# Kernel tuning notes

Measured on AMD Instinct MI355X. Metric: run time of the kernel, lower is better.

## Reference

```python
import jax, jax.numpy as jnp
import numpy as np

N = 12000   # atoms per side
K = 32      # neighbors per point per radius
E = N * K   # edges per radius
R = 1500    # residues per side
P = 4096    # correspondence pairs
LN_EPS = 1e-5


def setup_inputs() -> dict:
    rng = np.random.default_rng(0)

    def unit(v):
        return (v / np.linalg.norm(v, axis=-1, keepdims=True)).astype(np.float32)

    pos_A = (rng.standard_normal((N, 3)) * 10.0).astype(np.float32)
    pos_B = (rng.standard_normal((N, 3)) * 10.0).astype(np.float32)
    normal_A = unit(rng.standard_normal((N, 3)))
    normal_B = unit(rng.standard_normal((N, 3)))

    def make_edges():
        dst = np.repeat(np.arange(N), K)                      # every node is a target
        src = (dst + 1 + rng.integers(0, N - 1, size=dst.shape)) % N  # src != dst
        return np.stack([src, dst]).astype(np.int32)          # [2, E]

    edges_A = np.stack([make_edges() for _ in range(3)])      # [3, 2, E]
    edges_B = np.stack([make_edges() for _ in range(3)])

    residue_idx_A = (np.arange(N) // (N // R)).astype(np.int32)
    residue_idx_B = (np.arange(N) // (N // R)).astype(np.int32)
    src_idx = rng.integers(0, R, P).astype(np.int32)
    tgt_idx = rng.integers(0, R, P).astype(np.int32)

    g = lambda *s: (rng.standard_normal(s) * 0.2).astype(np.float32)
    inp = dict(
        pos_A=jnp.asarray(pos_A), normal_A=jnp.asarray(normal_A),
        pos_B=jnp.asarray(pos_B), normal_B=jnp.asarray(normal_B),
        edges_A=jnp.asarray(edges_A), edges_B=jnp.asarray(edges_B),
        residue_idx_A=jnp.asarray(residue_idx_A), residue_idx_B=jnp.asarray(residue_idx_B),
        src_idx=jnp.asarray(src_idx), tgt_idx=jnp.asarray(tgt_idx),
        num_res=R,
        conv_w1=jnp.asarray(g(3, 4, 4)), conv_b1=jnp.zeros((3, 4), jnp.float32),
        conv_g1=jnp.ones((3, 4), jnp.float32), conv_be1=jnp.zeros((3, 4), jnp.float32),
        conv_w2=jnp.asarray(g(3, 4, 128)), conv_b2=jnp.zeros((3, 128), jnp.float32),
        conv_g2=jnp.ones((3, 128), jnp.float32), conv_be2=jnp.zeros((3, 128), jnp.float32),
        atom_w=jnp.asarray(g(384, 512)) * 0.25, atom_b=jnp.zeros((512,), jnp.float32),
        atom_g=jnp.ones((512,), jnp.float32), atom_be=jnp.zeros((512,), jnp.float32),
        res_w=jnp.asarray(g(512, 512)) * 0.25, res_b=jnp.zeros((512,), jnp.float32),
        res_g=jnp.ones((512,), jnp.float32), res_be=jnp.zeros((512,), jnp.float32),
        lin1_w=jnp.asarray(g(512, 1)), lin1_b=jnp.zeros((1,), jnp.float32),
    )
    return inp


def _mlp_layer(x, w, b, g, be):
    # Seq(Linear, ReLU, LayerNorm, Dropout(eval)) from MLP()
    h = jax.nn.relu(x @ w + b)
    mu = jnp.mean(h, axis=-1, keepdims=True)
    var = jnp.mean((h - mu) ** 2, axis=-1, keepdims=True)
    return g * (h - mu) * jax.lax.rsqrt(var + LN_EPS) + be


def _angle(v1, v2):
    c = jnp.cross(v1, v2)
    return jnp.arctan2(jnp.linalg.norm(c, axis=-1), jnp.sum(v1 * v2, axis=-1))


def _ppf(pos, normal, src, dst):
    # PyG point_pair_features: [||d||, <(n_i,d), <(n_j,d), <(n_i,n_j)], d = pos_j - pos_i
    d = pos[src] - pos[dst]
    dist = jnp.linalg.norm(d, axis=-1)
    n_i, n_j = normal[dst], normal[src]
    return jnp.stack([dist, _angle(n_i, d), _angle(n_j, d), _angle(n_i, n_j)], axis=-1)  # [E,4]


def reference(pos_A, normal_A, pos_B, normal_B, edges_A, edges_B,
              residue_idx_A, residue_idx_B, src_idx, tgt_idx, num_res,
              conv_w1, conv_b1, conv_g1, conv_be1, conv_w2, conv_b2, conv_g2, conv_be2,
              atom_w, atom_b, atom_g, atom_be, res_w, res_b, res_g, res_be,
              lin1_w, lin1_b):
    n = pos_A.shape[0]

    def side(pos, normal, edges):
        feats = []
        for r in range(3):  # conv2, conv3, conv4 (shared across A/B sides)
            src, dst = edges[r, 0], edges[r, 1]
            f = _ppf(pos, normal, src, dst)                         # [E,4]
            h = _mlp_layer(f, conv_w1[r], conv_b1[r], conv_g1[r], conv_be1[r])
            h = _mlp_layer(h, conv_w2[r], conv_b2[r], conv_g2[r], conv_be2[r])  # [E,128]
            feats.append(jax.ops.segment_max(h, dst, num_segments=n))          # [N,128]
        x = jnp.concatenate(feats, axis=-1)                         # [N,384]
        return _mlp_layer(x, atom_w, atom_b, atom_g, atom_be)       # [N,512]

    atom_x_A = side(pos_A, normal_A, edges_A)
    atom_x_B = side(pos_B, normal_B, edges_B)

    res_x_A = jax.ops.segment_max(atom_x_A, residue_idx_A, num_segments=num_res)
    res_x_B = jax.ops.segment_max(atom_x_B, residue_idx_B, num_segments=num_res)
    res_x_A = _mlp_layer(res_x_A, res_w, res_b, res_g, res_be)
    res_x_B = _mlp_layer(res_x_B, res_w, res_b, res_g, res_be)

    x_s = res_x_A[src_idx]
    x_t = res_x_B[tgt_idx]
    out = (x_s - x_t) @ lin1_w + lin1_b                              # [P,1]
    return jax.nn.sigmoid(out)
```

## Files before the change

kernel.cpp:

```cpp
#include <hip/hip_runtime.h>
#include <hip/hip_bf16.h>
#include <math.h>

#define N_ATOMS 12000
#define K_NB 32
#define E_EDGES (N_ATOMS*K_NB)
#define R_RES 1500
#define P_PAIRS 4096
#define LN_EPS 1e-5f

typedef __attribute__((ext_vector_type(8))) short short8;
typedef __attribute__((ext_vector_type(4))) float f32x4;
typedef __attribute__((ext_vector_type(4))) unsigned int u32x4;

__device__ __forceinline__ f32x4 splat4(float v){ f32x4 r = {v,v,v,v}; return r; }

__device__ __forceinline__ unsigned short f2bf(float f){
  unsigned u = __builtin_bit_cast(unsigned, f);
  u += 0x7FFF + ((u >> 16) & 1);
  return (unsigned short)(u >> 16);
}

template<int CTRL>
__device__ __forceinline__ float dpp_add(float v){
  int x = __builtin_amdgcn_mov_dpp(__builtin_bit_cast(int, v), CTRL, 0xf, 0xf, true);
  return v + __builtin_bit_cast(float, x);
}
__device__ __forceinline__ float dpp16sum(float v){
  v = dpp_add<0xB1>(v);
  v = dpp_add<0x4E>(v);
  v = dpp_add<0x141>(v);
  v = dpp_add<0x140>(v);
  return v;
}

__device__ __forceinline__ float fast_atan2(float y, float x){
  float ax = fabsf(x);
  float mn = fminf(ax, y);
  float mx = fmaxf(fmaxf(ax, y), 1e-30f);
  float r  = __builtin_amdgcn_rcpf(mx);
  r = r * (2.0f - mx * r);
  float a = mn * r;
  float s = a * a;
  float p = -0.0117212f;
  p = fmaf(p, s,  0.05265332f);
  p = fmaf(p, s, -0.11643287f);
  p = fmaf(p, s,  0.19354346f);
  p = fmaf(p, s, -0.33262347f);
  p = fmaf(p, s,  0.99997726f);
  p = p * a;
  p = (y > ax) ? (1.57079632679f - p) : p;
  p = (x < 0.f) ? (3.14159265359f - p) : p;
  return p;
}

__device__ __forceinline__ float angle3(float ax,float ay,float az,
                                        float bx,float by,float bz){
  float cx = ay*bz - az*by;
  float cy = az*bx - ax*bz;
  float cz = ax*by - ay*bx;
  float cn = sqrtf(cx*cx + cy*cy + cz*cz);
  float dt = ax*bx + ay*by + az*bz;
  return fast_atan2(cn, dt);
}

__global__ __launch_bounds__(256) void geom_wpack_kernel(
    const float* __restrict__ pos_A, const float* __restrict__ nrm_A,
    const float* __restrict__ pos_B, const float* __restrict__ nrm_B,
    const int* __restrict__ edges_A, const int* __restrict__ edges_B,
    const float* __restrict__ w1, const float* __restrict__ b1,
    const float* __restrict__ g1, const float* __restrict__ be1,
    unsigned short* __restrict__ a_rec,
    const float* __restrict__ atom_w, const float* __restrict__ res_w,
    unsigned short* __restrict__ wpA, unsigned short* __restrict__ wpB)
{
  const int bx = blockIdx.x;
  const int r = blockIdx.y;
  const int side = blockIdx.z;

  if (bx >= 1500) {
    int fb = (r*2 + side)*299 + (bx - 1500);
    if (fb < 768) {
      int idx = fb*256 + threadIdx.x;
      int k = idx >> 9, n = idx & 511;
      wpA[(size_t)(k>>5)*512*32 + n*32 + (k&31)] = f2bf(atom_w[idx]);
    } else if (fb < 1792) {
      int idx = (fb - 768)*256 + threadIdx.x;
      int k = idx >> 9, n = idx & 511;
      wpB[(size_t)(k>>5)*512*32 + n*32 + (k&31)] = f2bf(res_w[idx]);
    }
    return;
  }

  const float* __restrict__ pos = side ? pos_B : pos_A;
  const float* __restrict__ nrm = side ? nrm_B : nrm_A;
  const int* __restrict__ edges = (side ? edges_B : edges_A) + r*(2*E_EDGES);

  const int e = bx*256 + threadIdx.x;
  const int src = edges[e];
  const int dst = e >> 5;

  float psx = pos[src*3+0], psy = pos[src*3+1], psz = pos[src*3+2];
  float pdx = pos[dst*3+0], pdy = pos[dst*3+1], pdz = pos[dst*3+2];
  float dx = psx-pdx, dy = psy-pdy, dz = psz-pdz;
  float nix = nrm[dst*3+0], niy = nrm[dst*3+1], niz = nrm[dst*3+2];
  float njx = nrm[src*3+0], njy = nrm[src*3+1], njz = nrm[src*3+2];

  float f0 = sqrtf(dx*dx + dy*dy + dz*dz);
  float f1 = angle3(nix,niy,niz, dx,dy,dz);
  float f2 = angle3(njx,njy,njz, dx,dy,dz);
  float f3 = angle3(nix,niy,niz, njx,njy,njz);

  const float* w1r  = w1 + r*16;
  const float* b1r  = b1 + r*4;
  const float* g1r  = g1 + r*4;
  const float* be1r = be1 + r*4;
  float h[4]; float s1 = 0.f;
  #pragma unroll
  for (int j = 0; j < 4; ++j) {
    float t = b1r[j] + f0*w1r[j] + f1*w1r[4+j] + f2*w1r[8+j] + f3*w1r[12+j];
    t = fmaxf(t, 0.f);
    h[j] = t; s1 += t;
  }
  float mu1 = s1*0.25f;
  float v1 = 0.f;
  #pragma unroll
  for (int j = 0; j < 4; ++j) { float d = h[j]-mu1; v1 += d*d; }
  float inv1 = rsqrtf(v1*0.25f + LN_EPS);
  float a0 = g1r[0]*(h[0]-mu1)*inv1 + be1r[0];
  float a1 = g1r[1]*(h[1]-mu1)*inv1 + be1r[1];
  float a2 = g1r[2]*(h[2]-mu1)*inv1 + be1r[2];
  float a3 = g1r[3]*(h[3]-mu1)*inv1 + be1r[3];

  ushort4 rec;
  rec.x = f2bf(a0); rec.y = f2bf(a1); rec.z = f2bf(a2); rec.w = f2bf(a3);
  *(ushort4*)(a_rec + ((size_t)(side*3+r)*E_EDGES + e)*4) = rec;
}

__global__ __launch_bounds__(256) void edge_gemm_kernel(
    const unsigned short* __restrict__ a_rec,
    const float* __restrict__ w2, const float* __restrict__ b2,
    const float* __restrict__ g2, const float* __restrict__ be2,
    unsigned short* __restrict__ feats_A, unsigned short* __restrict__ feats_B)
{
  const int r = blockIdx.y;
  const int side = blockIdx.z;
  unsigned short* __restrict__ feats = side ? feats_B : feats_A;

  const int tid  = threadIdx.x;
  const int wv   = tid >> 6;
  const int lane = tid & 63;
  const int l15  = lane & 15;
  const bool live = (lane < 16);

  const float* __restrict__ w2r = w2 + r*512;

  short8 bfrag[8];
  float bias[8], gg[8], ee[8];
  #pragma unroll
  for (int ct = 0; ct < 8; ++ct) {
    int n = ct*16 + l15;
    float v0 = w2r[0*128+n], v1 = w2r[1*128+n];
    float v2 = w2r[2*128+n], v3 = w2r[3*128+n];
    short8 bf = {0,0,0,0,0,0,0,0};
    bf[0] = live ? (short)f2bf(v0) : (short)0;
    bf[1] = live ? (short)f2bf(v1) : (short)0;
    bf[2] = live ? (short)f2bf(v2) : (short)0;
    bf[3] = live ? (short)f2bf(v3) : (short)0;
    bfrag[ct] = bf;
    bias[ct] = b2[r*128+n];
    gg[ct]   = g2[r*128+n];
    ee[ct]   = be2[r*128+n];
  }

  const int node0 = blockIdx.x*32 + wv*8;
  const unsigned short* __restrict__ arp0 =
      a_rec + ((size_t)(side*3+r)*E_EDGES + (size_t)node0*32)*4;

  const f32x4 zero4 = splat4(0.f);

  for (int nd = 0; nd < 8; ++nd) {
    const unsigned short* arp = arp0 + nd*32*4;
    ushort4 a4_0 = *(const ushort4*)(arp + (l15)*4);
    ushort4 a4_1 = *(const ushort4*)(arp + (16 + l15)*4);

    float nodemax[8];
    #pragma unroll
    for (int ct = 0; ct < 8; ++ct) nodemax[ct] = -3.4e38f;

    #pragma unroll
    for (int rt = 0; rt < 2; ++rt) {
      ushort4 a4 = rt ? a4_1 : a4_0;
      unsigned alo = (unsigned)a4.x | ((unsigned)a4.y << 16);
      unsigned ahi = (unsigned)a4.z | ((unsigned)a4.w << 16);
      alo = live ? alo : 0u;
      ahi = live ? ahi : 0u;
      u32x4 pk = {alo, ahi, 0u, 0u};
      short8 af = __builtin_bit_cast(short8, pk);

      f32x4 acc[8];
      #pragma unroll
      for (int ct = 0; ct < 8; ++ct)
        acc[ct] = __builtin_amdgcn_mfma_f32_16x16x32_bf16(af, bfrag[ct], zero4, 0, 0, 0);

      float p[4] = {0,0,0,0}, q[4] = {0,0,0,0};
      #pragma unroll
      for (int ct = 0; ct < 8; ++ct) {
        #pragma unroll
        for (int i = 0; i < 4; ++i) {
          float t = fmaxf(acc[ct][i] + bias[ct], 0.f);
          acc[ct][i] = t; p[i] += t; q[i] = fmaf(t, t, q[i]);
        }
      }
      #pragma unroll
      for (int i = 0; i < 4; ++i) {
        p[i] = dpp16sum(p[i]);
        q[i] = dpp16sum(q[i]);
      }
      float uu[4], vv[4];
      #pragma unroll
      for (int i = 0; i < 4; ++i) {
        float mu  = p[i]*(1.f/128.f);
        float var = fmaxf(q[i]*(1.f/128.f) - mu*mu, 0.f);
        float inv = rsqrtf(var + LN_EPS);
        uu[i] = inv; vv[i] = -mu*inv;
      }
      #pragma unroll
      for (int ct = 0; ct < 8; ++ct) {
        float vm = -3.4e38f;
        #pragma unroll
        for (int i = 0; i < 4; ++i) {
          float val = gg[ct]*fmaf(acc[ct][i], uu[i], vv[i]) + ee[ct];
          vm = fmaxf(vm, val);
        }
        nodemax[ct] = fmaxf(nodemax[ct], vm);
      }
    }

    #pragma unroll
    for (int ct = 0; ct < 8; ++ct) {
      float vm = nodemax[ct];
      vm = fmaxf(vm, __shfl_xor(vm, 16, 64));
      vm = fmaxf(vm, __shfl_xor(vm, 32, 64));
      nodemax[ct] = vm;
    }

    if (live) {
      const int gnode = node0 + nd;
      #pragma unroll
      for (int ct = 0; ct < 8; ++ct)
        feats[(size_t)gnode*384 + r*128 + ct*16 + l15] = f2bf(nodemax[ct]);
    }
  }
}

__global__ __launch_bounds__(256) void gemm_ln_kernel(
    const unsigned short* __restrict__ x_A, const unsigned short* __restrict__ x_B,
    const unsigned short* __restrict__ wp,
    const float* __restrict__ b, const float* __restrict__ g,
    const float* __restrict__ be,
    float* __restrict__ out_A, float* __restrict__ out_B,
    int nrows, int Kdim)
{
  const unsigned short* __restrict__ x = blockIdx.y ? x_B : x_A;
  float* __restrict__ out = blockIdx.y ? out_B : out_A;

  __shared__ __align__(16) unsigned short sA[64*40];
  __shared__ __align__(16) unsigned short sB[512*40];
  __shared__ float sb[512], sg[512], sbe[512];

  const int tid  = threadIdx.x;
  const int wv   = tid >> 6;
  const int lane = tid & 63;
  const int l15  = lane & 15;
  const int quad = lane >> 4;
  const int rbase = blockIdx.x * 64;

  sb[tid]      = b[tid];    sb[tid+256]  = b[tid+256];
  sg[tid]      = g[tid];    sg[tid+256]  = g[tid+256];
  sbe[tid]     = be[tid];   sbe[tid+256] = be[tid+256];

  const f32x4 zero4 = splat4(0.f);
  f32x4 acc[32];
  #pragma unroll
  for (int ct = 0; ct < 32; ++ct) acc[ct] = zero4;

  const int nchunk = Kdim >> 5;
  const int arow = tid >> 2, apart = tid & 3;
  int agr = rbase + arow; if (agr >= nrows) agr = nrows - 1;
  const unsigned short* aptr = x + (size_t)agr*Kdim + apart*8;

  for (int kc = 0; kc < nchunk; ++kc) {
    __syncthreads();
    *(float4*)&sA[arow*40 + apart*8] = *(const float4*)(aptr + kc*32);
    {
      const float4* src = (const float4*)(wp + (size_t)kc*512*32);
      #pragma unroll
      for (int i = 0; i < 8; ++i) {
        int fi = tid + i*256;
        int n = fi >> 2, part = fi & 3;
        *(float4*)&sB[n*40 + part*8] = src[fi];
      }
    }
    __syncthreads();
    short8 af = *(short8*)&sA[(wv*16 + l15)*40 + quad*8];
    #pragma unroll
    for (int ct = 0; ct < 32; ++ct) {
      short8 bf = *(short8*)&sB[(ct*16 + l15)*40 + quad*8];
      acc[ct] = __builtin_amdgcn_mfma_f32_16x16x32_bf16(af, bf, acc[ct], 0, 0, 0);
    }
  }

  f32x4 p = zero4, q = zero4;
  #pragma unroll
  for (int ct = 0; ct < 32; ++ct) {
    f32x4 t = __builtin_elementwise_max(acc[ct] + splat4(sb[ct*16 + l15]), zero4);
    acc[ct] = t;
    p += t;
    q += t * t;
  }
  #pragma unroll
  for (int i = 0; i < 4; ++i) {
    p[i] = dpp16sum(p[i]);
    q[i] = dpp16sum(q[i]);
  }
  f32x4 mu4  = p * splat4(1.f/512.f);
  f32x4 var4 = __builtin_elementwise_max(q * splat4(1.f/512.f) - mu4*mu4, zero4);
  f32x4 uu, vv;
  #pragma unroll
  for (int i = 0; i < 4; ++i) {
    float inv = rsqrtf(var4[i] + LN_EPS);
    uu[i] = inv; vv[i] = -mu4[i]*inv;
  }
  const int row0 = rbase + wv*16 + quad*4;
  #pragma unroll
  for (int ct = 0; ct < 32; ++ct) {
    int gcol = ct*16 + l15;
    f32x4 v = acc[ct]*uu + vv;
    v = splat4(sg[gcol])*v + splat4(sbe[gcol]);
    #pragma unroll
    for (int i = 0; i < 4; ++i) {
      int grow = row0 + i;
      if (grow < nrows)
        out[(size_t)grow*512 + gcol] = v[i];
    }
  }
}

__global__ __launch_bounds__(256) void gemm_ln_res_kernel(
    const float* __restrict__ ax_A, const float* __restrict__ ax_B,
    const unsigned short* __restrict__ wp,
    const float* __restrict__ b, const float* __restrict__ g,
    const float* __restrict__ be,
    float* __restrict__ out_A, float* __restrict__ out_B)
{
  const float* __restrict__ ax = blockIdx.y ? ax_B : ax_A;
  float* __restrict__ out = blockIdx.y ? out_B : out_A;

  __shared__ __align__(16) unsigned short sA[64*40];
  __shared__ __align__(16) unsigned short sB[512*40];
  __shared__ float sb[512], sg[512], sbe[512];

  const int tid  = threadIdx.x;
  const int wv   = tid >> 6;
  const int lane = tid & 63;
  const int l15  = lane & 15;
  const int quad = lane >> 4;
  const int rbase = blockIdx.x * 64;

  sb[tid]      = b[tid];    sb[tid+256]  = b[tid+256];
  sg[tid]      = g[tid];    sg[tid+256]  = g[tid+256];
  sbe[tid]     = be[tid];   sbe[tid+256] = be[tid+256];

  const f32x4 zero4 = splat4(0.f);
  f32x4 acc[32];
  #pragma unroll
  for (int ct = 0; ct < 32; ++ct) acc[ct] = zero4;

  const int arow = tid >> 2, apart = tid & 3;
  int rres = rbase + arow; if (rres >= R_RES) rres = R_RES - 1;
  const float* abase = ax + (size_t)rres*8*512 + apart*8;

  for (int kc = 0; kc < 16; ++kc) {
    __syncthreads();
    {
      const float* ap = abase + kc*32;
      float4 m0 = *(const float4*)(ap);
      float4 m1 = *(const float4*)(ap + 4);
      #pragma unroll
      for (int a = 1; a < 8; ++a) {
        float4 v0 = *(const float4*)(ap + (size_t)a*512);
        float4 v1 = *(const float4*)(ap + (size_t)a*512 + 4);
        m0.x = fmaxf(m0.x, v0.x); m0.y = fmaxf(m0.y, v0.y);
        m0.z = fmaxf(m0.z, v0.z); m0.w = fmaxf(m0.w, v0.w);
        m1.x = fmaxf(m1.x, v1.x); m1.y = fmaxf(m1.y, v1.y);
        m1.z = fmaxf(m1.z, v1.z); m1.w = fmaxf(m1.w, v1.w);
      }
      ushort4 o0, o1;
      o0.x = f2bf(m0.x); o0.y = f2bf(m0.y); o0.z = f2bf(m0.z); o0.w = f2bf(m0.w);
      o1.x = f2bf(m1.x); o1.y = f2bf(m1.y); o1.z = f2bf(m1.z); o1.w = f2bf(m1.w);
      *(ushort4*)&sA[arow*40 + apart*8]     = o0;
      *(ushort4*)&sA[arow*40 + apart*8 + 4] = o1;
    }
    {
      const float4* src = (const float4*)(wp + (size_t)kc*512*32);
      #pragma unroll
      for (int i = 0; i < 8; ++i) {
        int fi = tid + i*256;
        int n = fi >> 2, part = fi & 3;
        *(float4*)&sB[n*40 + part*8] = src[fi];
      }
    }
    __syncthreads();
    short8 af = *(short8*)&sA[(wv*16 + l15)*40 + quad*8];
    #pragma unroll
    for (int ct = 0; ct < 32; ++ct) {
      short8 bf = *(short8*)&sB[(ct*16 + l15)*40 + quad*8];
      acc[ct] = __builtin_amdgcn_mfma_f32_16x16x32_bf16(af, bf, acc[ct], 0, 0, 0);
    }
  }

  f32x4 p = zero4, q = zero4;
  #pragma unroll
  for (int ct = 0; ct < 32; ++ct) {
    f32x4 t = __builtin_elementwise_max(acc[ct] + splat4(sb[ct*16 + l15]), zero4);
    acc[ct] = t;
    p += t;
    q += t * t;
  }
  #pragma unroll
  for (int i = 0; i < 4; ++i) {
    p[i] = dpp16sum(p[i]);
    q[i] = dpp16sum(q[i]);
  }
  f32x4 mu4  = p * splat4(1.f/512.f);
  f32x4 var4 = __builtin_elementwise_max(q * splat4(1.f/512.f) - mu4*mu4, zero4);
  f32x4 uu, vv;
  #pragma unroll
  for (int i = 0; i < 4; ++i) {
    float inv = rsqrtf(var4[i] + LN_EPS);
    uu[i] = inv; vv[i] = -mu4[i]*inv;
  }
  const int row0 = rbase + wv*16 + quad*4;
  #pragma unroll
  for (int ct = 0; ct < 32; ++ct) {
    int gcol = ct*16 + l15;
    f32x4 v = acc[ct]*uu + vv;
    v = splat4(sg[gcol])*v + splat4(sbe[gcol]);
    #pragma unroll
    for (int i = 0; i < 4; ++i) {
      int grow = row0 + i;
      if (grow < R_RES)
        out[(size_t)grow*512 + gcol] = v[i];
    }
  }
}

__global__ __launch_bounds__(256) void final_kernel(
    const float* __restrict__ resx_A, const float* __restrict__ resx_B,
    const int* __restrict__ src_idx, const int* __restrict__ tgt_idx,
    const float* __restrict__ lin_w, const float* __restrict__ lin_b,
    float* __restrict__ outp)
{
  int p = blockIdx.x*256 + threadIdx.x;
  if (p >= P_PAIRS) return;
  const float4* xa = (const float4*)(resx_A + (size_t)src_idx[p]*512);
  const float4* xb = (const float4*)(resx_B + (size_t)tgt_idx[p]*512);
  const float4* wv = (const float4*)lin_w;
  float acc = 0.f;
  #pragma unroll 4
  for (int i = 0; i < 128; ++i) {
    float4 a = xa[i], b = xb[i], w = wv[i];
    acc += (a.x-b.x)*w.x + (a.y-b.y)*w.y + (a.z-b.z)*w.z + (a.w-b.w)*w.w;
  }
  acc += lin_b[0];
  outp[p] = 1.f/(1.f + expf(-acc));
}

extern "C" void kernel_launch(void* const* d_in, const int* in_sizes, int n_in,
                              void* d_out, int out_size, void* d_ws, size_t ws_size,
                              hipStream_t stream)
{
  const float* pos_A   = (const float*)d_in[0];
  const float* nrm_A   = (const float*)d_in[1];
  const float* pos_B   = (const float*)d_in[2];
  const float* nrm_B   = (const float*)d_in[3];
  const int*   edges_A = (const int*)d_in[4];
  const int*   edges_B = (const int*)d_in[5];
  const int*   src_idx = (const int*)d_in[8];
  const int*   tgt_idx = (const int*)d_in[9];
  const float* conv_w1  = (const float*)d_in[11];
  const float* conv_b1  = (const float*)d_in[12];
  const float* conv_g1  = (const float*)d_in[13];
  const float* conv_be1 = (const float*)d_in[14];
  const float* conv_w2  = (const float*)d_in[15];
  const float* conv_b2  = (const float*)d_in[16];
  const float* conv_g2  = (const float*)d_in[17];
  const float* conv_be2 = (const float*)d_in[18];
  const float* atom_w   = (const float*)d_in[19];
  const float* atom_b   = (const float*)d_in[20];
  const float* atom_g   = (const float*)d_in[21];
  const float* atom_be  = (const float*)d_in[22];
  const float* res_w    = (const float*)d_in[23];
  const float* res_b    = (const float*)d_in[24];
  const float* res_g    = (const float*)d_in[25];
  const float* res_be   = (const float*)d_in[26];
  const float* lin1_w   = (const float*)d_in[27];
  const float* lin1_b   = (const float*)d_in[28];

  unsigned short* feats_A = (unsigned short*)d_ws;
  unsigned short* feats_B = feats_A + (size_t)N_ATOMS*384;
  float* atomx_A = (float*)(feats_B + (size_t)N_ATOMS*384);
  float* atomx_B = atomx_A + (size_t)N_ATOMS*512;
  float* resx_A  = atomx_B + (size_t)N_ATOMS*512;
  float* resx_B  = resx_A + (size_t)R_RES*512;
  unsigned short* a_rec = (unsigned short*)(resx_B + (size_t)R_RES*512);
  unsigned short* wpA   = a_rec + (size_t)6*E_EDGES*4;
  unsigned short* wpB   = wpA + (size_t)384*512;

  dim3 gE(1500 + 299, 3, 2);
  geom_wpack_kernel<<<gE, 256, 0, stream>>>(pos_A, nrm_A, pos_B, nrm_B,
      edges_A, edges_B, conv_w1, conv_b1, conv_g1, conv_be1, a_rec,
      atom_w, res_w, wpA, wpB);

  dim3 gG(N_ATOMS/32, 3, 2);
  edge_gemm_kernel<<<gG, 256, 0, stream>>>(a_rec,
      conv_w2, conv_b2, conv_g2, conv_be2, feats_A, feats_B);

  dim3 gAtom((N_ATOMS + 63)/64, 2);
  gemm_ln_kernel<<<gAtom, 256, 0, stream>>>(feats_A, feats_B, wpA,
      atom_b, atom_g, atom_be, atomx_A, atomx_B, N_ATOMS, 384);

  dim3 gRes((R_RES + 63)/64, 2);
  gemm_ln_res_kernel<<<gRes, 256, 0, stream>>>(atomx_A, atomx_B, wpB,
      res_b, res_g, res_be, resx_A, resx_B);

  final_kernel<<<(P_PAIRS+255)/256, 256, 0, stream>>>(resx_A, resx_B,
      src_idx, tgt_idx, lin1_w, lin1_b, (float*)d_out);
}
```

Measured before the change: 357.5 us.

## Register-prefetch next K chunk in GEMM kernels and split final dot across lanes

Both GEMM+LayerNorm kernels now load the next K chunk of weights and activations into registers while the MFMA loop runs on the current chunk in shared memory. For the residue kernel this also covers the 8-way max pooling. This hides global-load latency behind the matrix math, at the cost of more registers per thread, which may lower occupancy. The final kernel spreads each pair's 512-wide dot product over 8 lanes that combine with shuffles, giving more parallelism and coalesced reads.

Result: slower. 378.0 us (+5.7%).

```diff
diff --git a/kernel.cpp b/kernel.cpp
--- a/kernel.cpp
+++ b/kernel.cpp
@@ -290,25 +290,36 @@
   int agr = rbase + arow; if (agr >= nrows) agr = nrows - 1;
   const unsigned short* aptr = x + (size_t)agr*Kdim + apart*8;
 
+  float4 breg[8];
+  {
+    const float4* src = (const float4*)(wp);
+    #pragma unroll
+    for (int i = 0; i < 8; ++i) breg[i] = src[tid + i*256];
+  }
+  float4 areg = *(const float4*)(aptr);
+
   for (int kc = 0; kc < nchunk; ++kc) {
+    *(float4*)&sA[arow*40 + apart*8] = areg;
+    #pragma unroll
+    for (int i = 0; i < 8; ++i) {
+      int fi = tid + i*256;
+      int n = fi >> 2, part = fi & 3;
+      *(float4*)&sB[n*40 + part*8] = breg[i];
+    }
     __syncthreads();
-    *(float4*)&sA[arow*40 + apart*8] = *(const float4*)(aptr + kc*32);
-    {
-      const float4* src = (const float4*)(wp + (size_t)kc*512*32);
-      #pragma unroll
-      for (int i = 0; i < 8; ++i) {
-        int fi = tid + i*256;
-        int n = fi >> 2, part = fi & 3;
-        *(float4*)&sB[n*40 + part*8] = src[fi];
-      }
-    }
-    __syncthreads();
+    if (kc + 1 < nchunk) {
+      const float4* src = (const float4*)(wp + (size_t)(kc+1)*512*32);
+      #pragma unroll
+      for (int i = 0; i < 8; ++i) breg[i] = src[tid + i*256];
+      areg = *(const float4*)(aptr + (kc+1)*32);
+    }
     short8 af = *(short8*)&sA[(wv*16 + l15)*40 + quad*8];
     #pragma unroll
     for (int ct = 0; ct < 32; ++ct) {
       short8 bf = *(short8*)&sB[(ct*16 + l15)*40 + quad*8];
       acc[ct] = __builtin_amdgcn_mfma_f32_16x16x32_bf16(af, bf, acc[ct], 0, 0, 0);
     }
+    __syncthreads();
   }
 
   f32x4 p = zero4, q = zero4;
@@ -381,43 +392,55 @@
   int rres = rbase + arow; if (rres >= R_RES) rres = R_RES - 1;
   const float* abase = ax + (size_t)rres*8*512 + apart*8;
 
+  auto amax_chunk = [&](int kc, ushort4& o0, ushort4& o1) {
+    const float* ap = abase + kc*32;
+    float4 m0 = *(const float4*)(ap);
+    float4 m1 = *(const float4*)(ap + 4);
+    #pragma unroll
+    for (int a = 1; a < 8; ++a) {
+      float4 v0 = *(const float4*)(ap + (size_t)a*512);
+      float4 v1 = *(const float4*)(ap + (size_t)a*512 + 4);
+      m0.x = fmaxf(m0.x, v0.x); m0.y = fmaxf(m0.y, v0.y);
+      m0.z = fmaxf(m0.z, v0.z); m0.w = fmaxf(m0.w, v0.w);
+      m1.x = fmaxf(m1.x, v1.x); m1.y = fmaxf(m1.y, v1.y);
+      m1.z = fmaxf(m1.z, v1.z); m1.w = fmaxf(m1.w, v1.w);
+    }
+    o0.x = f2bf(m0.x); o0.y = f2bf(m0.y); o0.z = f2bf(m0.z); o0.w = f2bf(m0.w);
+    o1.x = f2bf(m1.x); o1.y = f2bf(m1.y); o1.z = f2bf(m1.z); o1.w = f2bf(m1.w);
+  };
+
+  float4 breg[8];
+  {
+    const float4* src = (const float4*)(wp);
+    #pragma unroll
+    for (int i = 0; i < 8; ++i) breg[i] = src[tid + i*256];
+  }
+  ushort4 a0, a1;
+  amax_chunk(0, a0, a1);
+
   for (int kc = 0; kc < 16; ++kc) {
+    *(ushort4*)&sA[arow*40 + apart*8]     = a0;
+    *(ushort4*)&sA[arow*40 + apart*8 + 4] = a1;
+    #pragma unroll
+    for (int i = 0; i < 8; ++i) {
+      int fi = tid + i*256;
+      int n = fi >> 2, part = fi & 3;
+      *(float4*)&sB[n*40 + part*8] = breg[i];
+    }
     __syncthreads();
-    {
-      const float* ap = abase + kc*32;
-      float4 m0 = *(const float4*)(ap);
-      float4 m1 = *(const float4*)(ap + 4);
-      #pragma unroll
-      for (int a = 1; a < 8; ++a) {
-        float4 v0 = *(const float4*)(ap + (size_t)a*512);
-        float4 v1 = *(const float4*)(ap + (size_t)a*512 + 4);
-        m0.x = fmaxf(m0.x, v0.x); m0.y = fmaxf(m0.y, v0.y);
-        m0.z = fmaxf(m0.z, v0.z); m0.w = fmaxf(m0.w, v0.w);
-        m1.x = fmaxf(m1.x, v1.x); m1.y = fmaxf(m1.y, v1.y);
-        m1.z = fmaxf(m1.z, v1.z); m1.w = fmaxf(m1.w, v1.w);
-      }
-      ushort4 o0, o1;
-      o0.x = f2bf(m0.x); o0.y = f2bf(m0.y); o0.z = f2bf(m0.z); o0.w = f2bf(m0.w);
-      o1.x = f2bf(m1.x); o1.y = f2bf(m1.y); o1.z = f2bf(m1.z); o1.w = f2bf(m1.w);
-      *(ushort4*)&sA[arow*40 + apart*8]     = o0;
-      *(ushort4*)&sA[arow*40 + apart*8 + 4] = o1;
-    }
-    {
-      const float4* src = (const float4*)(wp + (size_t)kc*512*32);
-      #pragma unroll
-      for (int i = 0; i < 8; ++i) {
-        int fi = tid + i*256;
-        int n = fi >> 2, part = fi & 3;
-        *(float4*)&sB[n*40 + part*8] = src[fi];
-      }
-    }
-    __syncthreads();
+    if (kc + 1 < 16) {
+      const float4* src = (const float4*)(wp + (size_t)(kc+1)*512*32);
+      #pragma unroll
+      for (int i = 0; i < 8; ++i) breg[i] = src[tid + i*256];
+      amax_chunk(kc+1, a0, a1);
+    }
     short8 af = *(short8*)&sA[(wv*16 + l15)*40 + quad*8];
     #pragma unroll
     for (int ct = 0; ct < 32; ++ct) {
       short8 bf = *(short8*)&sB[(ct*16 + l15)*40 + quad*8];
       acc[ct] = __builtin_amdgcn_mfma_f32_16x16x32_bf16(af, bf, acc[ct], 0, 0, 0);
     }
+    __syncthreads();
   }
 
   f32x4 p = zero4, q = zero4;
@@ -462,19 +485,26 @@
     const float* __restrict__ lin_w, const float* __restrict__ lin_b,
     float* __restrict__ outp)
 {
-  int p = blockIdx.x*256 + threadIdx.x;
+  int idx = blockIdx.x*256 + threadIdx.x;
+  int p  = idx >> 3;
+  int l8 = idx & 7;
   if (p >= P_PAIRS) return;
-  const float4* xa = (const float4*)(resx_A + (size_t)src_idx[p]*512);
-  const float4* xb = (const float4*)(resx_B + (size_t)tgt_idx[p]*512);
-  const float4* wv = (const float4*)lin_w;
+  const float4* xa = (const float4*)(resx_A + (size_t)src_idx[p]*512) + l8;
+  const float4* xb = (const float4*)(resx_B + (size_t)tgt_idx[p]*512) + l8;
+  const float4* wv = (const float4*)lin_w + l8;
   float acc = 0.f;
-  #pragma unroll 4
-  for (int i = 0; i < 128; ++i) {
-    float4 a = xa[i], b = xb[i], w = wv[i];
+  #pragma unroll
+  for (int i = 0; i < 16; ++i) {
+    float4 a = xa[i*8], b = xb[i*8], w = wv[i*8];
     acc += (a.x-b.x)*w.x + (a.y-b.y)*w.y + (a.z-b.z)*w.z + (a.w-b.w)*w.w;
   }
-  acc += lin_b[0];
-  outp[p] = 1.f/(1.f + expf(-acc));
+  acc += __shfl_xor(acc, 1, 64);
+  acc += __shfl_xor(acc, 2, 64);
+  acc += __shfl_xor(acc, 4, 64);
+  if (l8 == 0) {
+    acc += lin_b[0];
+    outp[p] = 1.f/(1.f + expf(-acc));
+  }
 }
 
 extern "C" void kernel_launch(void* const* d_in, const int* in_sizes, int n_in,
@@ -535,6 +565,6 @@
   gemm_ln_res_kernel<<<gRes, 256, 0, stream>>>(atomx_A, atomx_B, wpB,
       res_b, res_g, res_be, resx_A, resx_B);
 
-  final_kernel<<<(P_PAIRS+255)/256, 256, 0, stream>>>(resx_A, resx_B,
+  final_kernel<<<(P_PAIRS*8 + 255)/256, 256, 0, stream>>>(resx_A, resx_B,
       src_idx, tgt_idx, lin1_w, lin1_b, (float*)d_out);
 }
```

## Fuse edge geometry into edge GEMM kernel and parallelize final dot product

Applied to the files above, without the earlier changes.

Edge features (PPF plus the first MLP layer) are now computed inside the edge GEMM kernel, with one lane per edge, and passed to the MFMA A-fragments through shuffles. This removes the a_rec intermediate written to and read back from global memory, along with one kernel launch. Weight packing moves into two separate small kernels. The final pair kernel splits each 512-wide dot product across 8 lanes and reduces with shuffles, adding parallelism to a kernel that previously ran one pair per thread.

Measured after the change: 324.0 us. 9.4% less time.

```diff
diff --git a/kernel.cpp b/kernel.cpp
--- a/kernel.cpp
+++ b/kernel.cpp
@@ -64,87 +64,30 @@
   return fast_atan2(cn, dt);
 }
 
-__global__ __launch_bounds__(256) void geom_wpack_kernel(
+__global__ __launch_bounds__(256) void wpack_kernel(
+    const float* __restrict__ w, unsigned short* __restrict__ wp, int Kdim)
+{
+  int idx = blockIdx.x*256 + threadIdx.x;
+  if (idx >= Kdim*512) return;
+  int k = idx >> 9, n = idx & 511;
+  wp[(size_t)(k>>5)*512*32 + n*32 + (k&31)] = f2bf(w[idx]);
+}
+
+__global__ __launch_bounds__(256) void edge_fused_kernel(
     const float* __restrict__ pos_A, const float* __restrict__ nrm_A,
     const float* __restrict__ pos_B, const float* __restrict__ nrm_B,
     const int* __restrict__ edges_A, const int* __restrict__ edges_B,
     const float* __restrict__ w1, const float* __restrict__ b1,
     const float* __restrict__ g1, const float* __restrict__ be1,
-    unsigned short* __restrict__ a_rec,
-    const float* __restrict__ atom_w, const float* __restrict__ res_w,
-    unsigned short* __restrict__ wpA, unsigned short* __restrict__ wpB)
-{
-  const int bx = blockIdx.x;
-  const int r = blockIdx.y;
-  const int side = blockIdx.z;
-
-  if (bx >= 1500) {
-    int fb = (r*2 + side)*299 + (bx - 1500);
-    if (fb < 768) {
-      int idx = fb*256 + threadIdx.x;
-      int k = idx >> 9, n = idx & 511;
-      wpA[(size_t)(k>>5)*512*32 + n*32 + (k&31)] = f2bf(atom_w[idx]);
-    } else if (fb < 1792) {
-      int idx = (fb - 768)*256 + threadIdx.x;
-      int k = idx >> 9, n = idx & 511;
-      wpB[(size_t)(k>>5)*512*32 + n*32 + (k&31)] = f2bf(res_w[idx]);
-    }
-    return;
-  }
-
-  const float* __restrict__ pos = side ? pos_B : pos_A;
-  const float* __restrict__ nrm = side ? nrm_B : nrm_A;
-  const int* __restrict__ edges = (side ? edges_B : edges_A) + r*(2*E_EDGES);
-
-  const int e = bx*256 + threadIdx.x;
-  const int src = edges[e];
-  const int dst = e >> 5;
-
-  float psx = pos[src*3+0], psy = pos[src*3+1], psz = pos[src*3+2];
-  float pdx = pos[dst*3+0], pdy = pos[dst*3+1], pdz = pos[dst*3+2];
-  float dx = psx-pdx, dy = psy-pdy, dz = psz-pdz;
-  float nix = nrm[dst*3+0], niy = nrm[dst*3+1], niz = nrm[dst*3+2];
-  float njx = nrm[src*3+0], njy = nrm[src*3+1], njz = nrm[src*3+2];
-
-  float f0 = sqrtf(dx*dx + dy*dy + dz*dz);
-  float f1 = angle3(nix,niy,niz, dx,dy,dz);
-  float f2 = angle3(njx,njy,njz, dx,dy,dz);
-  float f3 = angle3(nix,niy,niz, njx,njy,njz);
-
-  const float* w1r  = w1 + r*16;
-  const float* b1r  = b1 + r*4;
-  const float* g1r  = g1 + r*4;
-  const float* be1r = be1 + r*4;
-  float h[4]; float s1 = 0.f;
-  #pragma unroll
-  for (int j = 0; j < 4; ++j) {
-    float t = b1r[j] + f0*w1r[j] + f1*w1r[4+j] + f2*w1r[8+j] + f3*w1r[12+j];
-    t = fmaxf(t, 0.f);
-    h[j] = t; s1 += t;
-  }
-  float mu1 = s1*0.25f;
-  float v1 = 0.f;
-  #pragma unroll
-  for (int j = 0; j < 4; ++j) { float d = h[j]-mu1; v1 += d*d; }
-  float inv1 = rsqrtf(v1*0.25f + LN_EPS);
-  float a0 = g1r[0]*(h[0]-mu1)*inv1 + be1r[0];
-  float a1 = g1r[1]*(h[1]-mu1)*inv1 + be1r[1];
-  float a2 = g1r[2]*(h[2]-mu1)*inv1 + be1r[2];
-  float a3 = g1r[3]*(h[3]-mu1)*inv1 + be1r[3];
-
-  ushort4 rec;
-  rec.x = f2bf(a0); rec.y = f2bf(a1); rec.z = f2bf(a2); rec.w = f2bf(a3);
-  *(ushort4*)(a_rec + ((size_t)(side*3+r)*E_EDGES + e)*4) = rec;
-}
-
-__global__ __launch_bounds__(256) void edge_gemm_kernel(
-    const unsigned short* __restrict__ a_rec,
     const float* __restrict__ w2, const float* __restrict__ b2,
     const float* __restrict__ g2, const float* __restrict__ be2,
     unsigned short* __restrict__ feats_A, unsigned short* __restrict__ feats_B)
 {
   const int r = blockIdx.y;
   const int side = blockIdx.z;
+  const float* __restrict__ pos = side ? pos_B : pos_A;
+  const float* __restrict__ nrm = side ? nrm_B : nrm_A;
+  const int* __restrict__ edges = (side ? edges_B : edges_A) + r*(2*E_EDGES);
   unsigned short* __restrict__ feats = side ? feats_B : feats_A;
 
   const int tid  = threadIdx.x;
@@ -153,7 +96,11 @@
   const int l15  = lane & 15;
   const bool live = (lane < 16);
 
-  const float* __restrict__ w2r = w2 + r*512;
+  const float* __restrict__ w1r  = w1  + r*16;
+  const float* __restrict__ b1r  = b1  + r*4;
+  const float* __restrict__ g1r  = g1  + r*4;
+  const float* __restrict__ be1r = be1 + r*4;
+  const float* __restrict__ w2r  = w2  + r*512;
 
   short8 bfrag[8];
   float bias[8], gg[8], ee[8];
@@ -174,82 +121,113 @@
   }
 
   const int node0 = blockIdx.x*32 + wv*8;
-  const unsigned short* __restrict__ arp0 =
-      a_rec + ((size_t)(side*3+r)*E_EDGES + (size_t)node0*32)*4;
-
   const f32x4 zero4 = splat4(0.f);
 
-  for (int nd = 0; nd < 8; ++nd) {
-    const unsigned short* arp = arp0 + nd*32*4;
-    ushort4 a4_0 = *(const ushort4*)(arp + (l15)*4);
-    ushort4 a4_1 = *(const ushort4*)(arp + (16 + l15)*4);
-
-    float nodemax[8];
-    #pragma unroll
-    for (int ct = 0; ct < 8; ++ct) nodemax[ct] = -3.4e38f;
-
-    #pragma unroll
-    for (int rt = 0; rt < 2; ++rt) {
-      ushort4 a4 = rt ? a4_1 : a4_0;
-      unsigned alo = (unsigned)a4.x | ((unsigned)a4.y << 16);
-      unsigned ahi = (unsigned)a4.z | ((unsigned)a4.w << 16);
-      alo = live ? alo : 0u;
-      ahi = live ? ahi : 0u;
-      u32x4 pk = {alo, ahi, 0u, 0u};
-      short8 af = __builtin_bit_cast(short8, pk);
-
-      f32x4 acc[8];
+  for (int win = 0; win < 4; ++win) {
+    const int e = (node0 + win*2)*K_NB + lane;
+    const int src = edges[e];
+    const int dst = e >> 5;
+
+    float psx = pos[src*3+0], psy = pos[src*3+1], psz = pos[src*3+2];
+    float pdx = pos[dst*3+0], pdy = pos[dst*3+1], pdz = pos[dst*3+2];
+    float dx = psx-pdx, dy = psy-pdy, dz = psz-pdz;
+    float nix = nrm[dst*3+0], niy = nrm[dst*3+1], niz = nrm[dst*3+2];
+    float njx = nrm[src*3+0], njy = nrm[src*3+1], njz = nrm[src*3+2];
+
+    float f0 = sqrtf(dx*dx + dy*dy + dz*dz);
+    float f1 = angle3(nix,niy,niz, dx,dy,dz);
+    float f2 = angle3(njx,njy,njz, dx,dy,dz);
+    float f3 = angle3(nix,niy,niz, njx,njy,njz);
+
+    float h[4]; float s1 = 0.f;
+    #pragma unroll
+    for (int j = 0; j < 4; ++j) {
+      float t = b1r[j] + f0*w1r[j] + f1*w1r[4+j] + f2*w1r[8+j] + f3*w1r[12+j];
+      t = fmaxf(t, 0.f);
+      h[j] = t; s1 += t;
+    }
+    float mu1 = s1*0.25f;
+    float v1 = 0.f;
+    #pragma unroll
+    for (int j = 0; j < 4; ++j) { float d = h[j]-mu1; v1 += d*d; }
+    float inv1 = rsqrtf(v1*0.25f + LN_EPS);
+    float a0 = g1r[0]*(h[0]-mu1)*inv1 + be1r[0];
+    float a1 = g1r[1]*(h[1]-mu1)*inv1 + be1r[1];
+    float a2 = g1r[2]*(h[2]-mu1)*inv1 + be1r[2];
+    float a3 = g1r[3]*(h[3]-mu1)*inv1 + be1r[3];
+
+    unsigned alo = (unsigned)f2bf(a0) | ((unsigned)f2bf(a1) << 16);
+    unsigned ahi = (unsigned)f2bf(a2) | ((unsigned)f2bf(a3) << 16);
+
+    #pragma unroll
+    for (int nd2 = 0; nd2 < 2; ++nd2) {
+      float nodemax[8];
       #pragma unroll
-      for (int ct = 0; ct < 8; ++ct)
-        acc[ct] = __builtin_amdgcn_mfma_f32_16x16x32_bf16(af, bfrag[ct], zero4, 0, 0, 0);
-
-      float p[4] = {0,0,0,0}, q[4] = {0,0,0,0};
+      for (int ct = 0; ct < 8; ++ct) nodemax[ct] = -3.4e38f;
+
+      #pragma unroll
+      for (int rt = 0; rt < 2; ++rt) {
+        const int srcl = nd2*32 + rt*16 + l15;
+        unsigned palo = __shfl(alo, srcl, 64);
+        unsigned pahi = __shfl(ahi, srcl, 64);
+        palo = live ? palo : 0u;
+        pahi = live ? pahi : 0u;
+        u32x4 pk = {palo, pahi, 0u, 0u};
+        short8 af = __builtin_bit_cast(short8, pk);
+
+        f32x4 acc[8];
+        #pragma unroll
+        for (int ct = 0; ct < 8; ++ct)
+          acc[ct] = __builtin_amdgcn_mfma_f32_16x16x32_bf16(af, bfrag[ct], zero4, 0, 0, 0);
+
+        float p[4] = {0,0,0,0}, q[4] = {0,0,0,0};
+        #pragma unroll
+        for (int ct = 0; ct < 8; ++ct) {
+          #pragma unroll
+          for (int i = 0; i < 4; ++i) {
+            float t = fmaxf(acc[ct][i] + bias[ct], 0.f);
+            acc[ct][i] = t; p[i] += t; q[i] = fmaf(t, t, q[i]);
+          }
+        }
+        #pragma unroll
+        for (int i = 0; i < 4; ++i) {
+          p[i] = dpp16sum(p[i]);
+          q[i] = dpp16sum(q[i]);
+        }
+        float uu[4], vv[4];
+        #pragma unroll
+        for (int i = 0; i < 4; ++i) {
+          float mu  = p[i]*(1.f/128.f);
+          float var = fmaxf(q[i]*(1.f/128.f) - mu*mu, 0.f);
+          float inv = rsqrtf(var + LN_EPS);
+          uu[i] = inv; vv[i] = -mu*inv;
+        }
+        #pragma unroll
+        for (int ct = 0; ct < 8; ++ct) {
+          float vm = -3.4e38f;
+          #pragma unroll
+          for (int i = 0; i < 4; ++i) {
+            float val = gg[ct]*fmaf(acc[ct][i], uu[i], vv[i]) + ee[ct];
+            vm = fmaxf(vm, val);
+          }
+          nodemax[ct] = fmaxf(nodemax[ct], vm);
+        }
+      }
+
       #pragma unroll
       for (int ct = 0; ct < 8; ++ct) {
+        float vm = nodemax[ct];
+        vm = fmaxf(vm, __shfl_xor(vm, 16, 64));
+        vm = fmaxf(vm, __shfl_xor(vm, 32, 64));
+        nodemax[ct] = vm;
+      }
+
+      if (live) {
+        const int gnode = node0 + win*2 + nd2;
         #pragma unroll
-        for (int i = 0; i < 4; ++i) {
-          float t = fmaxf(acc[ct][i] + bias[ct], 0.f);
-          acc[ct][i] = t; p[i] += t; q[i] = fmaf(t, t, q[i]);
-        }
+        for (int ct = 0; ct < 8; ++ct)
+          feats[(size_t)gnode*384 + r*128 + ct*16 + l15] = f2bf(nodemax[ct]);
       }
-      #pragma unroll
-      for (int i = 0; i < 4; ++i) {
-        p[i] = dpp16sum(p[i]);
-        q[i] = dpp16sum(q[i]);
-      }
-      float uu[4], vv[4];
-      #pragma unroll
-      for (int i = 0; i < 4; ++i) {
-        float mu  = p[i]*(1.f/128.f);
-        float var = fmaxf(q[i]*(1.f/128.f) - mu*mu, 0.f);
-        float inv = rsqrtf(var + LN_EPS);
-        uu[i] = inv; vv[i] = -mu*inv;
-      }
-      #pragma unroll
-      for (int ct = 0; ct < 8; ++ct) {
-        float vm = -3.4e38f;
-        #pragma unroll
-        for (int i = 0; i < 4; ++i) {
-          float val = gg[ct]*fmaf(acc[ct][i], uu[i], vv[i]) + ee[ct];
-          vm = fmaxf(vm, val);
-        }
-        nodemax[ct] = fmaxf(nodemax[ct], vm);
-      }
-    }
-
-    #pragma unroll
-    for (int ct = 0; ct < 8; ++ct) {
-      float vm = nodemax[ct];
-      vm = fmaxf(vm, __shfl_xor(vm, 16, 64));
-      vm = fmaxf(vm, __shfl_xor(vm, 32, 64));
-      nodemax[ct] = vm;
-    }
-
-    if (live) {
-      const int gnode = node0 + nd;
-      #pragma unroll
-      for (int ct = 0; ct < 8; ++ct)
-        feats[(size_t)gnode*384 + r*128 + ct*16 + l15] = f2bf(nodemax[ct]);
     }
   }
 }
@@ -462,19 +440,26 @@
     const float* __restrict__ lin_w, const float* __restrict__ lin_b,
     float* __restrict__ outp)
 {
-  int p = blockIdx.x*256 + threadIdx.x;
+  int idx = blockIdx.x*256 + threadIdx.x;
+  int p  = idx >> 3;
+  int l8 = idx & 7;
   if (p >= P_PAIRS) return;
-  const float4* xa = (const float4*)(resx_A + (size_t)src_idx[p]*512);
-  const float4* xb = (const float4*)(resx_B + (size_t)tgt_idx[p]*512);
-  const float4* wv = (const float4*)lin_w;
+  const float4* xa = (const float4*)(resx_A + (size_t)src_idx[p]*512) + l8;
+  const float4* xb = (const float4*)(resx_B + (size_t)tgt_idx[p]*512) + l8;
+  const float4* wv = (const float4*)lin_w + l8;
   float acc = 0.f;
-  #pragma unroll 4
-  for (int i = 0; i < 128; ++i) {
-    float4 a = xa[i], b = xb[i], w = wv[i];
+  #pragma unroll
+  for (int i = 0; i < 16; ++i) {
+    float4 a = xa[i*8], b = xb[i*8], w = wv[i*8];
     acc += (a.x-b.x)*w.x + (a.y-b.y)*w.y + (a.z-b.z)*w.z + (a.w-b.w)*w.w;
   }
-  acc += lin_b[0];
-  outp[p] = 1.f/(1.f + expf(-acc));
+  acc += __shfl_xor(acc, 1, 64);
+  acc += __shfl_xor(acc, 2, 64);
+  acc += __shfl_xor(acc, 4, 64);
+  if (l8 == 0) {
+    acc += lin_b[0];
+    outp[p] = 1.f/(1.f + expf(-acc));
+  }
 }
 
 extern "C" void kernel_launch(void* const* d_in, const int* in_sizes, int n_in,
@@ -514,18 +499,18 @@
   float* atomx_B = atomx_A + (size_t)N_ATOMS*512;
   float* resx_A  = atomx_B + (size_t)N_ATOMS*512;
   float* resx_B  = resx_A + (size_t)R_RES*512;
-  unsigned short* a_rec = (unsigned short*)(resx_B + (size_t)R_RES*512);
-  unsigned short* wpA   = a_rec + (size_t)6*E_EDGES*4;
-  unsigned short* wpB   = wpA + (size_t)384*512;
-
-  dim3 gE(1500 + 299, 3, 2);
-  geom_wpack_kernel<<<gE, 256, 0, stream>>>(pos_A, nrm_A, pos_B, nrm_B,
-      edges_A, edges_B, conv_w1, conv_b1, conv_g1, conv_be1, a_rec,
-      atom_w, res_w, wpA, wpB);
+  unsigned short* wpA = (unsigned short*)(resx_B + (size_t)R_RES*512);
+  unsigned short* wpB = wpA + (size_t)384*512;
+
+  wpack_kernel<<<(384*512)/256, 256, 0, stream>>>(atom_w, wpA, 384);
+  wpack_kernel<<<(512*512)/256, 256, 0, stream>>>(res_w, wpB, 512);
 
   dim3 gG(N_ATOMS/32, 3, 2);
-  edge_gemm_kernel<<<gG, 256, 0, stream>>>(a_rec,
-      conv_w2, conv_b2, conv_g2, conv_be2, feats_A, feats_B);
+  edge_fused_kernel<<<gG, 256, 0, stream>>>(pos_A, nrm_A, pos_B, nrm_B,
+      edges_A, edges_B,
+      conv_w1, conv_b1, conv_g1, conv_be1,
+      conv_w2, conv_b2, conv_g2, conv_be2,
+      feats_A, feats_B);
 
   dim3 gAtom((N_ATOMS + 63)/64, 2);
   gemm_ln_kernel<<<gAtom, 256, 0, stream>>>(feats_A, feats_B, wpA,
@@ -535,6 +520,6 @@
   gemm_ln_res_kernel<<<gRes, 256, 0, stream>>>(atomx_A, atomx_B, wpB,
       res_b, res_g, res_be, resx_A, resx_B);
 
-  final_kernel<<<(P_PAIRS+255)/256, 256, 0, stream>>>(resx_A, resx_B,
+  final_kernel<<<(P_PAIRS*8 + 255)/256, 256, 0, stream>>>(resx_A, resx_B,
       src_idx, tgt_idx, lin1_w, lin1_b, (float*)d_out);
 }
```
